# Kernel tuning notes

Measured on AMD Instinct MI355X. Metric: run time of the kernel, lower is better.

## Reference

```python
import jax, jax.numpy as jnp
import numpy as np

N_NODES = 100000
N_EDGES = 1600000
IN_DIM = 4
HID = 64


def gcn_conv(x, src, dst, W, b, num_nodes):
    """PyG GCNConv: out = D^-1/2 (A+I) D^-1/2 (x @ W) + b, add aggregation."""
    loop = jnp.arange(num_nodes)
    src_f = jnp.concatenate([src, loop])  # [E+N]
    dst_f = jnp.concatenate([dst, loop])
    # degree from destination (col) counts, self loops included -> deg >= 1
    deg = jax.ops.segment_sum(jnp.ones_like(dst_f, dtype=x.dtype), dst_f,
                              num_segments=num_nodes)
    dinv = jax.lax.rsqrt(deg)
    norm = dinv[src_f] * dinv[dst_f]  # [E+N]
    h = x @ W  # [N, out] transform first (cheaper when out <= in is false too; matches PyG)
    msg = h[src_f] * norm[:, None]  # [E+N, out]
    out = jax.ops.segment_sum(msg, dst_f, num_segments=num_nodes)
    return out + b


def setup_inputs() -> dict:
    key = jax.random.key(0)
    ks = jax.random.split(key, 6)
    x = jax.random.normal(ks[0], (N_NODES, IN_DIM), dtype=jnp.float32)
    edge_index = jax.random.randint(ks[1], (2, N_EDGES), 0, N_NODES, dtype=jnp.int64)
    # glorot-ish scaled weights
    W1 = jax.random.normal(ks[2], (IN_DIM, HID), dtype=jnp.float32) / np.sqrt(IN_DIM)
    b1 = jnp.zeros((HID,), dtype=jnp.float32)
    W2 = jax.random.normal(ks[3], (HID, HID), dtype=jnp.float32) / np.sqrt(HID)
    b2 = jnp.zeros((HID,), dtype=jnp.float32)
    Wl = jax.random.normal(ks[4], (HID, 1), dtype=jnp.float32) / np.sqrt(HID)
    bl = jnp.zeros((1,), dtype=jnp.float32)
    return {"x": x, "edge_index": edge_index, "W1": W1, "b1": b1,
            "W2": W2, "b2": b2, "Wl": Wl, "bl": bl}


def reference(x, edge_index, W1, b1, W2, b2, Wl, bl):
    num_nodes = x.shape[0]
    src, dst = edge_index[0], edge_index[1]
    h = jax.nn.relu(gcn_conv(x, src, dst, W1, b1, num_nodes))
    h = jax.nn.relu(gcn_conv(h, src, dst, W2, b2, num_nodes))
    logits = (h @ Wl + bl).squeeze(-1)  # [N]
    return logits
```

## Files before the change

kernel.cpp:

```cpp
#include <hip/hip_runtime.h>

#define NN 100000
#define NE 1600000
#define HID 64
#define NBUK 391
#define SRCBITS 17
#define SRCMASK 0x1FFFF
#define EBLK 2048
#define GE2 ((NE + EBLK - 1) / EBLK)
#define SCANN (NBUK * GE2)
#define CHUNK 1024
#define NCH ((SCANN + CHUNK - 1) / CHUNK)

typedef __attribute__((ext_vector_type(8))) short bf16x8;
typedef __attribute__((ext_vector_type(4))) float f32x4;

__device__ __forceinline__ float bf2f(unsigned short u) {
    return __uint_as_float(((unsigned int)u) << 16);
}
__device__ __forceinline__ unsigned short f2bf(float f) {
    unsigned int x = __float_as_uint(f);
    return (unsigned short)((x + 0x7FFFu + ((x >> 16) & 1u)) >> 16);
}
__device__ __forceinline__ float bflo(unsigned int u) { return __uint_as_float(u << 16); }
__device__ __forceinline__ float bfhi(unsigned int u) { return __uint_as_float(u & 0xFFFF0000u); }

__device__ __forceinline__ int ld_idx(const int* __restrict__ ei, int off, int is64) {
    return is64 ? ei[2 * off] : ei[off];
}

__device__ __forceinline__ int detect_flag(const int* __restrict__ ei, int t, int* sflag) {
    if (t < 64) {
        unsigned long long b = __ballot(ei[2 * t + 1] != 0);
        if (t == 0) *sflag = (b == 0ULL) ? 1 : 0;
    }
    __syncthreads();
    return *sflag;
}

__global__ void k_histA(const int* __restrict__ ei, int* __restrict__ histG) {
    __shared__ int hist[NBUK];
    __shared__ int sflag;
    int t = threadIdx.x;
    for (int i = t; i < NBUK; i += 256) hist[i] = 0;
    int f = detect_flag(ei, t, &sflag);
    int base = blockIdx.x * EBLK;
#pragma unroll
    for (int k = 0; k < EBLK / 256; ++k) {
        int e = base + k * 256 + t;
        if (e < NE) {
            int d = ld_idx(ei, NE + e, f);
            atomicAdd(&hist[d >> 8], 1);
        }
    }
    __syncthreads();
    for (int i = t; i < NBUK; i += 256) histG[i * GE2 + blockIdx.x] = hist[i];
}

__global__ void k_scan1(int* __restrict__ g, int* __restrict__ bsum) {
    __shared__ int s[256];
    int t = threadIdx.x;
    int i4 = blockIdx.x * 256 + t;
    int base = i4 * 4;
    int4 v = make_int4(0, 0, 0, 0);
    if (base + 3 < SCANN) v = ((const int4*)g)[i4];
    else {
        if (base + 0 < SCANN) v.x = g[base + 0];
        if (base + 1 < SCANN) v.y = g[base + 1];
        if (base + 2 < SCANN) v.z = g[base + 2];
        if (base + 3 < SCANN) v.w = g[base + 3];
    }
    int tsum = v.x + v.y + v.z + v.w;
    s[t] = tsum; __syncthreads();
    for (int off = 1; off < 256; off <<= 1) {
        int u = (t >= off) ? s[t - off] : 0;
        __syncthreads();
        s[t] += u;
        __syncthreads();
    }
    int run = s[t] - tsum;
    int4 o;
    o.x = run; run += v.x;
    o.y = run; run += v.y;
    o.z = run; run += v.z;
    o.w = run;
    if (base + 3 < SCANN) ((int4*)g)[i4] = o;
    else {
        if (base + 0 < SCANN) g[base + 0] = o.x;
        if (base + 1 < SCANN) g[base + 1] = o.y;
        if (base + 2 < SCANN) g[base + 2] = o.z;
        if (base + 3 < SCANN) g[base + 3] = o.w;
    }
    if (t == 255) bsum[blockIdx.x] = s[255];
}

__global__ void k_scan2(int* __restrict__ bsum) {
    __shared__ int s[512];
    int t = threadIdx.x;
    int v = (t < NCH) ? bsum[t] : 0;
    s[t] = v; __syncthreads();
    for (int off = 1; off < 512; off <<= 1) {
        int u = (t >= off) ? s[t - off] : 0;
        __syncthreads();
        s[t] += u;
        __syncthreads();
    }
    if (t < NCH) bsum[t] = s[t] - v;
}

__global__ void k_scan3(int* __restrict__ g, const int* __restrict__ bsum) {
    int t = threadIdx.x;
    int i4 = blockIdx.x * 256 + t;
    int base = i4 * 4;
    int add = bsum[blockIdx.x];
    if (base + 3 < SCANN) {
        int4 v = ((const int4*)g)[i4];
        v.x += add; v.y += add; v.z += add; v.w += add;
        ((int4*)g)[i4] = v;
    } else {
        if (base + 0 < SCANN) g[base + 0] += add;
        if (base + 1 < SCANN) g[base + 1] += add;
        if (base + 2 < SCANN) g[base + 2] += add;
        if (base + 3 < SCANN) g[base + 3] += add;
    }
}

__global__ void k_fillA(const int* __restrict__ ei, const int* __restrict__ histS,
                        unsigned int* __restrict__ bbuf) {
    __shared__ int cur[NBUK];
    __shared__ int sflag;
    int t = threadIdx.x;
    for (int i = t; i < NBUK; i += 256) cur[i] = histS[i * GE2 + blockIdx.x];
    int f = detect_flag(ei, t, &sflag);
    int base = blockIdx.x * EBLK;
#pragma unroll
    for (int k = 0; k < EBLK / 256; ++k) {
        int e = base + k * 256 + t;
        if (e < NE) {
            int s = ld_idx(ei, e, f);
            int d = ld_idx(ei, NE + e, f);
            int p = atomicAdd(&cur[d >> 8], 1);
            bbuf[p] = ((unsigned int)(d & 255) << SRCBITS) | (unsigned int)s;
        }
    }
}

__global__ void k_passB(const unsigned int* __restrict__ bbuf, const int* __restrict__ histS,
                        const float* __restrict__ x,
                        int* __restrict__ cnt, int* __restrict__ offs,
                        float* __restrict__ dinv, float* __restrict__ xs,
                        int* __restrict__ csr) {
    __shared__ int hist[256];
    __shared__ int scn[256];
    __shared__ int cur[256];
    int t = threadIdx.x;
    int b = blockIdx.x;
    int base = histS[b * GE2];
    int next = (b == NBUK - 1) ? NE : histS[(b + 1) * GE2];
    int sz = next - base;
    const unsigned int* buf = bbuf + base;
    hist[t] = 0;
    __syncthreads();
    for (int e = t; e < sz; e += 256)
        atomicAdd(&hist[buf[e] >> SRCBITS], 1);
    __syncthreads();
    int deg = hist[t];
    scn[t] = deg; __syncthreads();
    for (int off = 1; off < 256; off <<= 1) {
        int u = (t >= off) ? scn[t - off] : 0;
        __syncthreads();
        scn[t] += u;
        __syncthreads();
    }
    int myoff = base + scn[t] - deg;
    int node = b * 256 + t;
    if (node < NN) {
        cnt[node]  = deg;
        offs[node] = myoff;
        float d = 1.0f / sqrtf((float)(deg + 1));
        dinv[node] = d;
        float4 xv = ((const float4*)x)[node];
        float4 o; o.x = d * xv.x; o.y = d * xv.y; o.z = d * xv.z; o.w = d * xv.w;
        ((float4*)xs)[node] = o;
    }
    cur[t] = myoff;
    __syncthreads();
    for (int e = t; e < sz; e += 256) {
        unsigned int u = buf[e];
        int p = atomicAdd(&cur[u >> SRCBITS], 1);
        csr[p] = (int)(u & SRCMASK);
    }
}

__global__ void k_agg1(const float* __restrict__ x, const float* __restrict__ xs,
                       const float* __restrict__ dinv, const int* __restrict__ offs,
                       const int* __restrict__ cnt, const int* __restrict__ csr,
                       float* __restrict__ agg) {
    int i = blockIdx.x * 256 + threadIdx.x;
    if (i >= NN) return;
    float sx = 0.f, sy = 0.f, sz = 0.f, sw = 0.f;
    int b = offs[i], n = cnt[i];
    int j = 0;
    for (; j + 8 <= n; j += 8) {
        int s0 = csr[b + j + 0], s1 = csr[b + j + 1], s2 = csr[b + j + 2], s3 = csr[b + j + 3];
        int s4 = csr[b + j + 4], s5 = csr[b + j + 5], s6 = csr[b + j + 6], s7 = csr[b + j + 7];
        float4 v0 = ((const float4*)xs)[s0];
        float4 v1 = ((const float4*)xs)[s1];
        float4 v2 = ((const float4*)xs)[s2];
        float4 v3 = ((const float4*)xs)[s3];
        float4 v4 = ((const float4*)xs)[s4];
        float4 v5 = ((const float4*)xs)[s5];
        float4 v6 = ((const float4*)xs)[s6];
        float4 v7 = ((const float4*)xs)[s7];
        sx += v0.x + v1.x + v2.x + v3.x + v4.x + v5.x + v6.x + v7.x;
        sy += v0.y + v1.y + v2.y + v3.y + v4.y + v5.y + v6.y + v7.y;
        sz += v0.z + v1.z + v2.z + v3.z + v4.z + v5.z + v6.z + v7.z;
        sw += v0.w + v1.w + v2.w + v3.w + v4.w + v5.w + v6.w + v7.w;
    }
    for (; j < n; ++j) {
        int s = csr[b + j];
        float4 v = ((const float4*)xs)[s];
        sx += v.x; sy += v.y; sz += v.z; sw += v.w;
    }
    float d = dinv[i];
    float4 xi = ((const float4*)x)[i];
    float4 o;
    o.x = d * (sx + d * xi.x);
    o.y = d * (sy + d * xi.y);
    o.z = d * (sz + d * xi.z);
    o.w = d * (sw + d * xi.w);
    ((float4*)agg)[i] = o;
}

__global__ void k_mm(const float* __restrict__ agg, const float* __restrict__ W1,
                     const float* __restrict__ b1, const float* __restrict__ W2,
                     const float* __restrict__ dinv, unsigned short* __restrict__ hs) {
    __shared__ unsigned short h1b[64 * 72];
    __shared__ unsigned short w2t[64 * 72];
    __shared__ float4 sAgg[64];
    __shared__ float sW1[256];
    __shared__ float sb1[64];
    __shared__ float sDinv[64];
    int t = threadIdx.x;
    int base = blockIdx.x * 64;
    if (t < 64) {
        int g = base + t;
        sAgg[t]  = (g < NN) ? ((const float4*)agg)[g] : make_float4(0.f, 0.f, 0.f, 0.f);
        sDinv[t] = (g < NN) ? dinv[g] : 0.f;
        sb1[t]   = b1[t];
    }
    sW1[t] = W1[t];
    for (int i = t; i < 4096; i += 256) {
        int k = i >> 6, n = i & 63;
        w2t[n * 72 + k] = f2bf(W2[i]);
    }
    if (blockIdx.x == 0 && t >= 128 && t < 192) hs[NN * 64 + (t - 128)] = 0;
    __syncthreads();
#pragma unroll
    for (int i = 0; i < 16; ++i) {
        int e = t + i * 256;
        int nl = e >> 6, c = e & 63;
        float4 a = sAgg[nl];
        float h = fmaf(a.x, sW1[c], fmaf(a.y, sW1[64 + c],
                  fmaf(a.z, sW1[128 + c], fmaf(a.w, sW1[192 + c], sb1[c]))));
        h1b[nl * 72 + c] = f2bf(fmaxf(h, 0.f));
    }
    __syncthreads();
    int w = t >> 6, lane = t & 63, l15 = lane & 15, quad = lane >> 4;
    bf16x8 a0 = *(const bf16x8*)&h1b[(w * 16 + l15) * 72 + quad * 8];
    bf16x8 a1 = *(const bf16x8*)&h1b[(w * 16 + l15) * 72 + 32 + quad * 8];
    f32x4 acc[4];
#pragma unroll
    for (int nt = 0; nt < 4; ++nt) {
        bf16x8 bb0 = *(const bf16x8*)&w2t[(nt * 16 + l15) * 72 + quad * 8];
        bf16x8 bb1 = *(const bf16x8*)&w2t[(nt * 16 + l15) * 72 + 32 + quad * 8];
        f32x4 c = {0.f, 0.f, 0.f, 0.f};
        c = __builtin_amdgcn_mfma_f32_16x16x32_bf16(a0, bb0, c, 0, 0, 0);
        c = __builtin_amdgcn_mfma_f32_16x16x32_bf16(a1, bb1, c, 0, 0, 0);
        acc[nt] = c;
    }
#pragma unroll
    for (int nt = 0; nt < 4; ++nt) {
#pragma unroll
        for (int r = 0; r < 4; ++r) {
            int localn = w * 16 + quad * 4 + r;
            int g = base + localn;
            if (g < NN) hs[g * 64 + nt * 16 + l15] = f2bf(acc[nt][r] * sDinv[localn]);
        }
    }
}

__global__ void k_gather_head(const unsigned short* __restrict__ hs, const int* __restrict__ offs,
                              const int* __restrict__ cnt, const int* __restrict__ csr,
                              const float* __restrict__ dinv, const float* __restrict__ b2,
                              const float* __restrict__ Wl, const float* __restrict__ bl,
                              float* __restrict__ out) {
    int t = threadIdx.x;
    int node = blockIdx.x * 4 + (t >> 6);
    int c = t & 63;
    int qg = c >> 4;
    int ql = c & 15;
    int b = offs[node], n = cnt[node];
    const uint2* hrow = (const uint2*)hs;
    int myidx = (c < n) ? csr[b + c] : NN;
    int m = n < 64 ? n : 64;
    float4 A = make_float4(0.f, 0.f, 0.f, 0.f);
    float4 B = make_float4(0.f, 0.f, 0.f, 0.f);
    for (int j = 0; j < m; j += 16) {
        int s0 = __shfl(myidx, j + qg, 64);
        int s1 = __shfl(myidx, j + 4 + qg, 64);
        int s2 = __shfl(myidx, j + 8 + qg, 64);
        int s3 = __shfl(myidx, j + 12 + qg, 64);
        uint2 u0 = hrow[s0 * 16 + ql];
        uint2 u1 = hrow[s1 * 16 + ql];
        uint2 u2 = hrow[s2 * 16 + ql];
        uint2 u3 = hrow[s3 * 16 + ql];
        A.x += bflo(u0.x); A.y += bfhi(u0.x); A.z += bflo(u0.y); A.w += bfhi(u0.y);
        B.x += bflo(u1.x); B.y += bfhi(u1.x); B.z += bflo(u1.y); B.w += bfhi(u1.y);
        A.x += bflo(u2.x); A.y += bfhi(u2.x); A.z += bflo(u2.y); A.w += bfhi(u2.y);
        B.x += bflo(u3.x); B.y += bfhi(u3.x); B.z += bflo(u3.y); B.w += bfhi(u3.y);
    }
    for (int j = 64; j < n; j += 4) {
        int e = j + qg;
        int s = (e < n) ? csr[b + e] : NN;
        uint2 u = hrow[s * 16 + ql];
        A.x += bflo(u.x); A.y += bfhi(u.x); A.z += bflo(u.y); A.w += bfhi(u.y);
    }
    float4 S;
    S.x = A.x + B.x; S.y = A.y + B.y; S.z = A.z + B.z; S.w = A.w + B.w;
    S.x += __shfl_xor(S.x, 16, 64); S.x += __shfl_xor(S.x, 32, 64);
    S.y += __shfl_xor(S.y, 16, 64); S.y += __shfl_xor(S.y, 32, 64);
    S.z += __shfl_xor(S.z, 16, 64); S.z += __shfl_xor(S.z, 32, 64);
    S.w += __shfl_xor(S.w, 16, 64); S.w += __shfl_xor(S.w, 32, 64);
    uint2 uS = hrow[node * 16 + ql];
    S.x += bflo(uS.x); S.y += bfhi(uS.x); S.z += bflo(uS.y); S.w += bfhi(uS.y);
    float4 bv = ((const float4*)b2)[ql];
    float4 wv = ((const float4*)Wl)[ql];
    float dn = dinv[node];
    float v = fmaxf(fmaf(dn, S.x, bv.x), 0.f) * wv.x
            + fmaxf(fmaf(dn, S.y, bv.y), 0.f) * wv.y
            + fmaxf(fmaf(dn, S.z, bv.z), 0.f) * wv.z
            + fmaxf(fmaf(dn, S.w, bv.w), 0.f) * wv.w;
#pragma unroll
    for (int off = 8; off; off >>= 1) v += __shfl_down(v, off, 16);
    if (c == 0) out[node] = v + bl[0];
}

extern "C" void kernel_launch(void* const* d_in, const int* in_sizes, int n_in,
                              void* d_out, int out_size, void* d_ws, size_t ws_size,
                              hipStream_t stream) {
    const float* x  = (const float*)d_in[0];
    const int*   ei = (const int*)d_in[1];
    const float* W1 = (const float*)d_in[2];
    const float* b1 = (const float*)d_in[3];
    const float* W2 = (const float*)d_in[4];
    const float* b2 = (const float*)d_in[5];
    const float* Wl = (const float*)d_in[6];
    const float* bl = (const float*)d_in[7];
    float* out = (float*)d_out;

    char* w = (char*)d_ws;
    float* dinv  = (float*)w;                  w += NN * 4;
    int*   cnt   = (int*)w;                    w += NN * 4;
    int*   offs  = (int*)w;                    w += NN * 4;
    int*   csr   = (int*)w;                    w += NE * 4;
    float* xs    = (float*)w;                  w += NN * 4 * 4;
    float* agg   = (float*)w;                  w += NN * 4 * 4;
    unsigned short* hs = (unsigned short*)w;   w += (size_t)(NN + 1) * HID * 2;
    int*   histG = (int*)w;                    w += (size_t)((SCANN + 3) & ~3) * 4;
    int*   bsum  = (int*)w;                    w += 512 * 4;
    unsigned int* bbuf = (unsigned int*)w;     w += (size_t)NE * 4;

    const int GN = (NN + 255) / 256;
    const int GMM = (NN + 63) / 64;

    hipLaunchKernelGGL(k_histA,  dim3(GE2),  dim3(256), 0, stream, ei, histG);
    hipLaunchKernelGGL(k_scan1,  dim3(NCH),  dim3(256), 0, stream, histG, bsum);
    hipLaunchKernelGGL(k_scan2,  dim3(1),    dim3(512), 0, stream, bsum);
    hipLaunchKernelGGL(k_scan3,  dim3(NCH),  dim3(256), 0, stream, histG, bsum);
    hipLaunchKernelGGL(k_fillA,  dim3(GE2),  dim3(256), 0, stream, ei, histG, bbuf);
    hipLaunchKernelGGL(k_passB,  dim3(NBUK), dim3(256), 0, stream,
                       bbuf, histG, x, cnt, offs, dinv, xs, csr);

    hipLaunchKernelGGL(k_agg1, dim3(GN), dim3(256), 0, stream,
                       x, xs, dinv, offs, cnt, csr, agg);
    hipLaunchKernelGGL(k_mm, dim3(GMM), dim3(256), 0, stream,
                       agg, W1, b1, W2, dinv, hs);
    hipLaunchKernelGGL(k_gather_head, dim3(NN / 4), dim3(256), 0, stream,
                       hs, offs, cnt, csr, dinv, b2, Wl, bl, out);
}
```

Before: 184.5 us.

## Fuse layer-1 aggregation into matmul kernel and fold scan fixup into consumers

Removes the k_scan3 pass by having k_fillA and k_passB add the per-chunk block sum on the fly when reading scanned histogram offsets. Fuses the first-layer neighbor aggregation into the matmul kernel, using four threads per node to gather source features into shared memory before the W1/W2 transform. This drops two launches and the agg intermediate buffer round-trip. In exchange, the gather now runs inside the MFMA kernel, with more shared memory per block and 64 nodes per 256 threads.

Result: faster. 180.2 us (-2.3%).

```diff
diff --git a/kernel.cpp b/kernel.cpp
--- a/kernel.cpp
+++ b/kernel.cpp
@@ -108,29 +108,15 @@
     if (t < NCH) bsum[t] = s[t] - v;
 }
 
-__global__ void k_scan3(int* __restrict__ g, const int* __restrict__ bsum) {
-    int t = threadIdx.x;
-    int i4 = blockIdx.x * 256 + t;
-    int base = i4 * 4;
-    int add = bsum[blockIdx.x];
-    if (base + 3 < SCANN) {
-        int4 v = ((const int4*)g)[i4];
-        v.x += add; v.y += add; v.z += add; v.w += add;
-        ((int4*)g)[i4] = v;
-    } else {
-        if (base + 0 < SCANN) g[base + 0] += add;
-        if (base + 1 < SCANN) g[base + 1] += add;
-        if (base + 2 < SCANN) g[base + 2] += add;
-        if (base + 3 < SCANN) g[base + 3] += add;
-    }
-}
-
 __global__ void k_fillA(const int* __restrict__ ei, const int* __restrict__ histS,
-                        unsigned int* __restrict__ bbuf) {
+                        const int* __restrict__ bsum, unsigned int* __restrict__ bbuf) {
     __shared__ int cur[NBUK];
     __shared__ int sflag;
     int t = threadIdx.x;
-    for (int i = t; i < NBUK; i += 256) cur[i] = histS[i * GE2 + blockIdx.x];
+    for (int i = t; i < NBUK; i += 256) {
+        int idx = i * GE2 + blockIdx.x;
+        cur[i] = histS[idx] + bsum[idx >> 10];
+    }
     int f = detect_flag(ei, t, &sflag);
     int base = blockIdx.x * EBLK;
 #pragma unroll
@@ -146,7 +132,7 @@
 }
 
 __global__ void k_passB(const unsigned int* __restrict__ bbuf, const int* __restrict__ histS,
-                        const float* __restrict__ x,
+                        const int* __restrict__ bsum, const float* __restrict__ x,
                         int* __restrict__ cnt, int* __restrict__ offs,
                         float* __restrict__ dinv, float* __restrict__ xs,
                         int* __restrict__ csr) {
@@ -155,8 +141,9 @@
     __shared__ int cur[256];
     int t = threadIdx.x;
     int b = blockIdx.x;
-    int base = histS[b * GE2];
-    int next = (b == NBUK - 1) ? NE : histS[(b + 1) * GE2];
+    int i0 = b * GE2;
+    int base = histS[i0] + bsum[i0 >> 10];
+    int next = (b == NBUK - 1) ? NE : (histS[i0 + GE2] + bsum[(i0 + GE2) >> 10]);
     int sz = next - base;
     const unsigned int* buf = bbuf + base;
     hist[t] = 0;
@@ -192,62 +179,31 @@
     }
 }
 
-__global__ void k_agg1(const float* __restrict__ x, const float* __restrict__ xs,
-                       const float* __restrict__ dinv, const int* __restrict__ offs,
-                       const int* __restrict__ cnt, const int* __restrict__ csr,
-                       float* __restrict__ agg) {
-    int i = blockIdx.x * 256 + threadIdx.x;
-    if (i >= NN) return;
-    float sx = 0.f, sy = 0.f, sz = 0.f, sw = 0.f;
-    int b = offs[i], n = cnt[i];
-    int j = 0;
-    for (; j + 8 <= n; j += 8) {
-        int s0 = csr[b + j + 0], s1 = csr[b + j + 1], s2 = csr[b + j + 2], s3 = csr[b + j + 3];
-        int s4 = csr[b + j + 4], s5 = csr[b + j + 5], s6 = csr[b + j + 6], s7 = csr[b + j + 7];
-        float4 v0 = ((const float4*)xs)[s0];
-        float4 v1 = ((const float4*)xs)[s1];
-        float4 v2 = ((const float4*)xs)[s2];
-        float4 v3 = ((const float4*)xs)[s3];
-        float4 v4 = ((const float4*)xs)[s4];
-        float4 v5 = ((const float4*)xs)[s5];
-        float4 v6 = ((const float4*)xs)[s6];
-        float4 v7 = ((const float4*)xs)[s7];
-        sx += v0.x + v1.x + v2.x + v3.x + v4.x + v5.x + v6.x + v7.x;
-        sy += v0.y + v1.y + v2.y + v3.y + v4.y + v5.y + v6.y + v7.y;
-        sz += v0.z + v1.z + v2.z + v3.z + v4.z + v5.z + v6.z + v7.z;
-        sw += v0.w + v1.w + v2.w + v3.w + v4.w + v5.w + v6.w + v7.w;
-    }
-    for (; j < n; ++j) {
-        int s = csr[b + j];
-        float4 v = ((const float4*)xs)[s];
-        sx += v.x; sy += v.y; sz += v.z; sw += v.w;
-    }
-    float d = dinv[i];
-    float4 xi = ((const float4*)x)[i];
-    float4 o;
-    o.x = d * (sx + d * xi.x);
-    o.y = d * (sy + d * xi.y);
-    o.z = d * (sz + d * xi.z);
-    o.w = d * (sw + d * xi.w);
-    ((float4*)agg)[i] = o;
-}
-
-__global__ void k_mm(const float* __restrict__ agg, const float* __restrict__ W1,
-                     const float* __restrict__ b1, const float* __restrict__ W2,
-                     const float* __restrict__ dinv, unsigned short* __restrict__ hs) {
+__global__ void k_mm2(const float* __restrict__ xs, const int* __restrict__ cnt,
+                      const int* __restrict__ offs, const int* __restrict__ csr,
+                      const float* __restrict__ dinv,
+                      const float* __restrict__ W1, const float* __restrict__ b1,
+                      const float* __restrict__ W2, unsigned short* __restrict__ hs) {
     __shared__ unsigned short h1b[64 * 72];
     __shared__ unsigned short w2t[64 * 72];
+    __shared__ float4 sPart[256];
     __shared__ float4 sAgg[64];
+    __shared__ float4 sXs[64];
     __shared__ float sW1[256];
     __shared__ float sb1[64];
-    __shared__ float sDinv[64];
+    __shared__ float sdv[64];
+    __shared__ int scnt[64];
+    __shared__ int soff[64];
     int t = threadIdx.x;
     int base = blockIdx.x * 64;
     if (t < 64) {
         int g = base + t;
-        sAgg[t]  = (g < NN) ? ((const float4*)agg)[g] : make_float4(0.f, 0.f, 0.f, 0.f);
-        sDinv[t] = (g < NN) ? dinv[g] : 0.f;
-        sb1[t]   = b1[t];
+        bool ok = (g < NN);
+        scnt[t] = ok ? cnt[g] : 0;
+        soff[t] = ok ? offs[g] : 0;
+        sdv[t]  = ok ? dinv[g] : 0.f;
+        sXs[t]  = ok ? ((const float4*)xs)[g] : make_float4(0.f, 0.f, 0.f, 0.f);
+        sb1[t]  = b1[t];
     }
     sW1[t] = W1[t];
     for (int i = t; i < 4096; i += 256) {
@@ -256,9 +212,41 @@
     }
     if (blockIdx.x == 0 && t >= 128 && t < 192) hs[NN * 64 + (t - 128)] = 0;
     __syncthreads();
+    {
+        int node_l = t & 63, part = t >> 6;
+        int n = scnt[node_l], b0 = soff[node_l];
+        float4 s = make_float4(0.f, 0.f, 0.f, 0.f);
+        int j = part;
+        for (; j + 8 <= n; j += 8) {
+            int s0 = csr[b0 + j], s1 = csr[b0 + j + 4];
+            float4 v0 = ((const float4*)xs)[s0];
+            float4 v1 = ((const float4*)xs)[s1];
+            s.x += v0.x + v1.x; s.y += v0.y + v1.y;
+            s.z += v0.z + v1.z; s.w += v0.w + v1.w;
+        }
+        for (; j < n; j += 4) {
+            int s0 = csr[b0 + j];
+            float4 v = ((const float4*)xs)[s0];
+            s.x += v.x; s.y += v.y; s.z += v.z; s.w += v.w;
+        }
+        sPart[t] = s;
+    }
+    __syncthreads();
+    if (t < 64) {
+        float4 a = sPart[t], b = sPart[t + 64], c = sPart[t + 128], d = sPart[t + 192];
+        float4 xi = sXs[t];
+        float dn = sdv[t];
+        float4 o;
+        o.x = dn * (a.x + b.x + c.x + d.x + xi.x);
+        o.y = dn * (a.y + b.y + c.y + d.y + xi.y);
+        o.z = dn * (a.z + b.z + c.z + d.z + xi.z);
+        o.w = dn * (a.w + b.w + c.w + d.w + xi.w);
+        sAgg[t] = o;
+    }
+    __syncthreads();
 #pragma unroll
     for (int i = 0; i < 16; ++i) {
-        int e = t + i * 256;
+        int e = i * 256 + t;
         int nl = e >> 6, c = e & 63;
         float4 a = sAgg[nl];
         float h = fmaf(a.x, sW1[c], fmaf(a.y, sW1[64 + c],
@@ -285,7 +273,7 @@
         for (int r = 0; r < 4; ++r) {
             int localn = w * 16 + quad * 4 + r;
             int g = base + localn;
-            if (g < NN) hs[g * 64 + nt * 16 + l15] = f2bf(acc[nt][r] * sDinv[localn]);
+            if (g < NN) hs[g * 64 + nt * 16 + l15] = f2bf(acc[nt][r] * sdv[localn]);
         }
     }
 }
@@ -365,27 +353,21 @@
     int*   offs  = (int*)w;                    w += NN * 4;
     int*   csr   = (int*)w;                    w += NE * 4;
     float* xs    = (float*)w;                  w += NN * 4 * 4;
-    float* agg   = (float*)w;                  w += NN * 4 * 4;
     unsigned short* hs = (unsigned short*)w;   w += (size_t)(NN + 1) * HID * 2;
     int*   histG = (int*)w;                    w += (size_t)((SCANN + 3) & ~3) * 4;
     int*   bsum  = (int*)w;                    w += 512 * 4;
     unsigned int* bbuf = (unsigned int*)w;     w += (size_t)NE * 4;
 
-    const int GN = (NN + 255) / 256;
     const int GMM = (NN + 63) / 64;
 
     hipLaunchKernelGGL(k_histA,  dim3(GE2),  dim3(256), 0, stream, ei, histG);
     hipLaunchKernelGGL(k_scan1,  dim3(NCH),  dim3(256), 0, stream, histG, bsum);
     hipLaunchKernelGGL(k_scan2,  dim3(1),    dim3(512), 0, stream, bsum);
-    hipLaunchKernelGGL(k_scan3,  dim3(NCH),  dim3(256), 0, stream, histG, bsum);
-    hipLaunchKernelGGL(k_fillA,  dim3(GE2),  dim3(256), 0, stream, ei, histG, bbuf);
+    hipLaunchKernelGGL(k_fillA,  dim3(GE2),  dim3(256), 0, stream, ei, histG, bsum, bbuf);
     hipLaunchKernelGGL(k_passB,  dim3(NBUK), dim3(256), 0, stream,
-                       bbuf, histG, x, cnt, offs, dinv, xs, csr);
-
-    hipLaunchKernelGGL(k_agg1, dim3(GN), dim3(256), 0, stream,
-                       x, xs, dinv, offs, cnt, csr, agg);
-    hipLaunchKernelGGL(k_mm, dim3(GMM), dim3(256), 0, stream,
-                       agg, W1, b1, W2, dinv, hs);
+                       bbuf, histG, bsum, x, cnt, offs, dinv, xs, csr);
+    hipLaunchKernelGGL(k_mm2, dim3(GMM), dim3(256), 0, stream,
+                       xs, cnt, offs, csr, dinv, W1, b1, W2, hs);
     hipLaunchKernelGGL(k_gather_head, dim3(NN / 4), dim3(256), 0, stream,
                        hs, offs, cnt, csr, dinv, b2, Wl, bl, out);
 }
```
